# Kernel tuning notes

Measured on AMD Instinct MI355X. Metric: run time of the kernel, lower is better.

The kernel has to match this reference:

```python
import jax, jax.numpy as jnp
import numpy as np
from jax import lax

# dims: batch, seq len, views, d_model; d_state, d_inner=2*d_model, d_conv, dt_rank=ceil(d_model/16)
B, L, V, D = 4, 512, 4, 256
DS, DI, DCONV, DTR = 16, 512, 4, 16
EPS = 1e-5

def setup_inputs():
    key = jax.random.key(0)
    ks = jax.random.split(key, 10)
    rn = lambda k, s, sc: jax.random.normal(k, s, jnp.float32) * sc
    return {
        "x": rn(ks[0], (B, L, V, D), 1.0),
        "ln_g": jnp.ones((V, D), jnp.float32),
        "ln_b": jnp.zeros((V, D), jnp.float32),
        "w_in": rn(ks[1], (V, 2 * DI, D), D ** -0.5),
        "conv_w": rn(ks[2], (V, DI, DCONV), DCONV ** -0.5),
        "conv_b": rn(ks[3], (V, DI), 0.02),
        "w_x": rn(ks[4], (V, DTR + 2 * DS, DI), DI ** -0.5),
        "w_dt": rn(ks[5], (V, DI, DTR), DTR ** -0.5),
        "b_dt": rn(ks[6], (V, DI), 0.02),
        "A_log": rn(ks[7], (V, DI, DS), 0.5),
        "D_skip": jnp.ones((V, DI), jnp.float32),
        "w_out": rn(ks[8], (V, D, DI), DI ** -0.5),
    }

def _layernorm(x, g, b):
    mu = x.mean(-1, keepdims=True)
    var = ((x - mu) ** 2).mean(-1, keepdims=True)
    return (x - mu) * lax.rsqrt(var + EPS) * g + b

def _mamba_view(xv, w_in, conv_w, conv_b, w_x, w_dt, b_dt, A_log, D_skip, w_out):
    # xv: (B, L, D)
    xz = jnp.einsum('bld,ed->ble', xv, w_in)            # (B, L, 2*DI)
    xi, z = xz[..., :DI], xz[..., DI:]
    # causal depthwise conv over time
    xt = jnp.moveaxis(xi, 1, 2)                          # (B, DI, L)
    xt = jnp.pad(xt, ((0, 0), (0, 0), (DCONV - 1, 0)))
    xc = lax.conv_general_dilated(xt, conv_w[:, None, :], (1,), 'VALID',
                                  feature_group_count=DI,
                                  dimension_numbers=('NCH', 'OIH', 'NCH'))
    xc = jax.nn.silu(xc + conv_b[None, :, None])
    xc = jnp.moveaxis(xc, 1, 2)                          # (B, L, DI)
    xdbl = jnp.einsum('bld,ed->ble', xc, w_x)            # (B, L, DTR+2*DS)
    dt_lo = xdbl[..., :DTR]
    Bc = xdbl[..., DTR:DTR + DS]
    Cc = xdbl[..., DTR + DS:]
    delta = jax.nn.softplus(jnp.einsum('blr,dr->bld', dt_lo, w_dt) + b_dt)
    A = -jnp.exp(A_log)                                  # (DI, DS)
    dA = jnp.exp(jnp.einsum('bld,dn->bldn', delta, A))   # discretized A
    dBu = jnp.einsum('bld,bln,bld->bldn', delta, Bc, xc) # discretized B*u

    def step(h, inp):
        dA_t, dBu_t, C_t = inp
        h = dA_t * h + dBu_t                             # (B, DI, DS)
        return h, jnp.einsum('bdn,bn->bd', h, C_t)

    h0 = jnp.zeros((B, DI, DS), xv.dtype)
    _, ys = lax.scan(step, h0, (jnp.moveaxis(dA, 1, 0), jnp.moveaxis(dBu, 1, 0), jnp.moveaxis(Cc, 1, 0)))
    y = jnp.moveaxis(ys, 0, 1) + xc * D_skip             # (B, L, DI)
    y = y * jax.nn.silu(z)
    return jnp.einsum('bld,od->blo', y, w_out)           # (B, L, D)

def _forward(x, ln_g, ln_b, w_in, conv_w, conv_b, w_x, w_dt, b_dt, A_log, D_skip, w_out):
    xv = jnp.moveaxis(x, 2, 0)                           # (V, B, L, D)
    def per_view(xv_i, g, b, wi, cw, cb, wx, wdt, bdt, al, dsk, wo):
        return _mamba_view(_layernorm(xv_i, g, b), wi, cw, cb, wx, wdt, bdt, al, dsk, wo)
    outs = jax.vmap(per_view)(xv, ln_g, ln_b, w_in, conv_w, conv_b, w_x, w_dt, b_dt, A_log, D_skip, w_out)
    return jnp.moveaxis(outs, 0, 2)                      # (B, L, V, D)

def reference(x, ln_g, ln_b, w_in, conv_w, conv_b, w_x, w_dt, b_dt, A_log, D_skip, w_out):
    # eval mode: view_mask == ones, dropout identity, gather is None -> h == agents
    agents = _forward(x, ln_g, ln_b, w_in, conv_w, conv_b, w_x, w_dt, b_dt, A_log, D_skip, w_out)
    return (agents, agents)
```

## Files before the change

### kernel.cpp

```cpp
#include <hip/hip_runtime.h>
#include <hip/hip_bf16.h>
#include <math.h>

#define B_ 4
#define L_ 512
#define V_ 4
#define D_ 256
#define DS_ 16
#define DI_ 512
#define DTR_ 16
#define ML (B_*L_)
#define NC_ 16
#define CL_ 32

#define OFF_RA   0
#define SZ_RA    ((long)V_*ML*D_)
#define OFF_XZ   (OFF_RA + SZ_RA)
#define SZ_XZ    ((long)V_*ML*2*DI_)
#define OFF_XC   (OFF_XZ + SZ_XZ)
#define SZ_XC    ((long)V_*ML*DI_)
#define OFF_XDBL (OFF_XC + SZ_XC)
#define SZ_XDBL  ((long)V_*ML*48)
#define OFF_SDEL (OFF_XDBL + SZ_XDBL)
#define SZ_SDEL  ((long)V_*B_*NC_*DI_)

typedef short short8_t __attribute__((ext_vector_type(8)));
typedef float f32x4_t  __attribute__((ext_vector_type(4)));

__device__ __forceinline__ float silu_f(float x) { return x / (1.f + expf(-x)); }
__device__ __forceinline__ ushort f2bf(float f) {
    uint u = __float_as_uint(f);
    return (ushort)((u + 0x7fffu + ((u >> 16) & 1u)) >> 16);
}
__device__ __forceinline__ float bf2f(ushort h) { return __uint_as_float(((uint)h) << 16); }

__global__ __launch_bounds__(256) void split_w(const float* __restrict__ in,
                                               ushort* __restrict__ oh,
                                               ushort* __restrict__ ol, int n4)
{
    const int i = blockIdx.x*256 + threadIdx.x;
    if (i >= n4) return;
    const float4 f = ((const float4*)in)[i];
    const ushort h0=f2bf(f.x), h1=f2bf(f.y), h2=f2bf(f.z), h3=f2bf(f.w);
    ((short4*)oh)[i] = make_short4((short)h0,(short)h1,(short)h2,(short)h3);
    ((short4*)ol)[i] = make_short4((short)f2bf(f.x-bf2f(h0)), (short)f2bf(f.y-bf2f(h1)),
                                   (short)f2bf(f.z-bf2f(h2)), (short)f2bf(f.w-bf2f(h3)));
}

__global__ __launch_bounds__(256) void ln_split(const float* __restrict__ x,
                                                const float* __restrict__ g,
                                                const float* __restrict__ bta,
                                                ushort* __restrict__ xh,
                                                ushort* __restrict__ xl)
{
    const int m = blockIdx.x;
    const int v = blockIdx.y;
    const int d = threadIdx.x;
    const float val = x[((long)m*V_ + v)*D_ + d];
    float s = val, sq = val*val;
#pragma unroll
    for (int off = 32; off >= 1; off >>= 1) {
        s  += __shfl_xor(s, off);
        sq += __shfl_xor(sq, off);
    }
    __shared__ float ws[4], wq[4];
    if ((threadIdx.x & 63) == 0) { ws[threadIdx.x >> 6] = s; wq[threadIdx.x >> 6] = sq; }
    __syncthreads();
    s  = ws[0]+ws[1]+ws[2]+ws[3];
    sq = wq[0]+wq[1]+wq[2]+wq[3];
    const float mu  = s * (1.f/D_);
    const float var = sq * (1.f/D_) - mu*mu;
    const float inv = rsqrtf(var + 1e-5f);
    const float r = (val - mu)*inv*g[v*D_+d] + bta[v*D_+d];
    const ushort h = f2bf(r);
    const long idx = ((long)v*ML + m)*D_ + d;
    xh[idx] = h;
    xl[idx] = f2bf(r - bf2f(h));
}

__global__ __launch_bounds__(256,2) void mfma_gemm_in(
    const ushort* __restrict__ Ah, const ushort* __restrict__ Al,
    const ushort* __restrict__ Bh, const ushort* __restrict__ Bl,
    float* __restrict__ C)
{
    const int v = blockIdx.z;
    const long Ao = (long)v*ML*D_;
    const long Bo = (long)v*(2*DI_)*D_;
    C += (long)v*ML*(2*DI_);
    const int bm = blockIdx.y*128, bn = blockIdx.x*128;
    __shared__ ushort sAh[128][40], sAl[128][40], sBh[128][40], sBl[128][40];
    const int tid  = threadIdx.x;
    const int lane = tid & 63, w = tid >> 6;
    const int wr = w >> 1, wc = w & 1;
    const int fm = lane & 15, fg = lane >> 4;
    const int r = tid >> 1, q0 = (tid & 1)*2;

    f32x4_t acc[4][4];
#pragma unroll
    for (int i=0;i<4;++i)
#pragma unroll
        for (int j=0;j<4;++j)
#pragma unroll
            for (int k=0;k<4;++k) acc[i][j][k]=0.f;

    const ushort* Agh = Ah + Ao + (long)(bm+r)*D_ + q0*8;
    const ushort* Agl = Al + Ao + (long)(bm+r)*D_ + q0*8;
    const ushort* Bgh = Bh + Bo + (long)(bn+r)*D_ + q0*8;
    const ushort* Bgl = Bl + Bo + (long)(bn+r)*D_ + q0*8;

    for (int k0 = 0; k0 < D_; k0 += 32) {
        const uint4 a0 = *(const uint4*)(Agh + k0);
        const uint4 a1 = *(const uint4*)(Agh + k0 + 8);
        const uint4 a2 = *(const uint4*)(Agl + k0);
        const uint4 a3 = *(const uint4*)(Agl + k0 + 8);
        const uint4 b0 = *(const uint4*)(Bgh + k0);
        const uint4 b1 = *(const uint4*)(Bgh + k0 + 8);
        const uint4 b2 = *(const uint4*)(Bgl + k0);
        const uint4 b3 = *(const uint4*)(Bgl + k0 + 8);
        __syncthreads();
        *(uint4*)&sAh[r][q0*8]   = a0;  *(uint4*)&sAh[r][q0*8+8] = a1;
        *(uint4*)&sAl[r][q0*8]   = a2;  *(uint4*)&sAl[r][q0*8+8] = a3;
        *(uint4*)&sBh[r][q0*8]   = b0;  *(uint4*)&sBh[r][q0*8+8] = b1;
        *(uint4*)&sBl[r][q0*8]   = b2;  *(uint4*)&sBl[r][q0*8+8] = b3;
        __syncthreads();
        short8_t ah[4], al[4], bh[4], bl[4];
#pragma unroll
        for (int i=0;i<4;++i) {
            ah[i] = *(const short8_t*)&sAh[wr*64 + i*16 + fm][fg*8];
            al[i] = *(const short8_t*)&sAl[wr*64 + i*16 + fm][fg*8];
            bh[i] = *(const short8_t*)&sBh[wc*64 + i*16 + fm][fg*8];
            bl[i] = *(const short8_t*)&sBl[wc*64 + i*16 + fm][fg*8];
        }
#pragma unroll
        for (int i=0;i<4;++i)
#pragma unroll
            for (int j=0;j<4;++j) {
                acc[i][j] = __builtin_amdgcn_mfma_f32_16x16x32_bf16(ah[i], bh[j], acc[i][j], 0,0,0);
                acc[i][j] = __builtin_amdgcn_mfma_f32_16x16x32_bf16(ah[i], bl[j], acc[i][j], 0,0,0);
                acc[i][j] = __builtin_amdgcn_mfma_f32_16x16x32_bf16(al[i], bh[j], acc[i][j], 0,0,0);
            }
    }
#pragma unroll
    for (int i=0;i<4;++i)
#pragma unroll
        for (int j4=0;j4<4;++j4) {
            const int row = bm + wr*64 + i*16 + fg*4 + j4;
            float* cr = C + (long)row*(2*DI_) + bn + wc*64 + fm;
#pragma unroll
            for (int j=0;j<4;++j) cr[j*16] = acc[i][j][j4];
        }
}

__global__ __launch_bounds__(256,2) void mfma_gemm_out(
    const uint* __restrict__ Apk,
    const ushort* __restrict__ Bh, const ushort* __restrict__ Bl,
    float* __restrict__ Cout)
{
    const int v = blockIdx.z;
    Apk += (long)v*ML*DI_;
    const long Bo = (long)v*D_*DI_;
    const int bm = blockIdx.y*128, bn = blockIdx.x*128;
    __shared__ ushort sAh[128][40], sAl[128][40], sBh[128][40], sBl[128][40];
    const int tid  = threadIdx.x;
    const int lane = tid & 63, w = tid >> 6;
    const int wr = w >> 1, wc = w & 1;
    const int fm = lane & 15, fg = lane >> 4;
    const int r = tid >> 1, hh = tid & 1, q0 = (tid & 1)*2;

    f32x4_t acc[4][4];
#pragma unroll
    for (int i=0;i<4;++i)
#pragma unroll
        for (int j=0;j<4;++j)
#pragma unroll
            for (int k=0;k<4;++k) acc[i][j][k]=0.f;

    const uint*   Ag  = Apk + (long)(bm+r)*DI_ + hh*16;
    const ushort* Bgh = Bh + Bo + (long)(bn+r)*DI_ + q0*8;
    const ushort* Bgl = Bl + Bo + (long)(bn+r)*DI_ + q0*8;

    for (int k0 = 0; k0 < DI_; k0 += 32) {
        const uint4 p0 = *(const uint4*)(Ag + k0);
        const uint4 p1 = *(const uint4*)(Ag + k0 + 4);
        const uint4 p2 = *(const uint4*)(Ag + k0 + 8);
        const uint4 p3 = *(const uint4*)(Ag + k0 + 12);
        const uint4 b0 = *(const uint4*)(Bgh + k0);
        const uint4 b1 = *(const uint4*)(Bgh + k0 + 8);
        const uint4 b2 = *(const uint4*)(Bgl + k0);
        const uint4 b3 = *(const uint4*)(Bgl + k0 + 8);
        __syncthreads();
        *(short4*)&sAh[r][hh*16+ 0] = make_short4((short)(p0.x&0xffff),(short)(p0.y&0xffff),(short)(p0.z&0xffff),(short)(p0.w&0xffff));
        *(short4*)&sAl[r][hh*16+ 0] = make_short4((short)(p0.x>>16),(short)(p0.y>>16),(short)(p0.z>>16),(short)(p0.w>>16));
        *(short4*)&sAh[r][hh*16+ 4] = make_short4((short)(p1.x&0xffff),(short)(p1.y&0xffff),(short)(p1.z&0xffff),(short)(p1.w&0xffff));
        *(short4*)&sAl[r][hh*16+ 4] = make_short4((short)(p1.x>>16),(short)(p1.y>>16),(short)(p1.z>>16),(short)(p1.w>>16));
        *(short4*)&sAh[r][hh*16+ 8] = make_short4((short)(p2.x&0xffff),(short)(p2.y&0xffff),(short)(p2.z&0xffff),(short)(p2.w&0xffff));
        *(short4*)&sAl[r][hh*16+ 8] = make_short4((short)(p2.x>>16),(short)(p2.y>>16),(short)(p2.z>>16),(short)(p2.w>>16));
        *(short4*)&sAh[r][hh*16+12] = make_short4((short)(p3.x&0xffff),(short)(p3.y&0xffff),(short)(p3.z&0xffff),(short)(p3.w&0xffff));
        *(short4*)&sAl[r][hh*16+12] = make_short4((short)(p3.x>>16),(short)(p3.y>>16),(short)(p3.z>>16),(short)(p3.w>>16));
        *(uint4*)&sBh[r][q0*8]   = b0;  *(uint4*)&sBh[r][q0*8+8] = b1;
        *(uint4*)&sBl[r][q0*8]   = b2;  *(uint4*)&sBl[r][q0*8+8] = b3;
        __syncthreads();
        short8_t ah[4], al[4], bh[4], bl[4];
#pragma unroll
        for (int i=0;i<4;++i) {
            ah[i] = *(const short8_t*)&sAh[wr*64 + i*16 + fm][fg*8];
            al[i] = *(const short8_t*)&sAl[wr*64 + i*16 + fm][fg*8];
            bh[i] = *(const short8_t*)&sBh[wc*64 + i*16 + fm][fg*8];
            bl[i] = *(const short8_t*)&sBl[wc*64 + i*16 + fm][fg*8];
        }
#pragma unroll
        for (int i=0;i<4;++i)
#pragma unroll
            for (int j=0;j<4;++j) {
                acc[i][j] = __builtin_amdgcn_mfma_f32_16x16x32_bf16(ah[i], bh[j], acc[i][j], 0,0,0);
                acc[i][j] = __builtin_amdgcn_mfma_f32_16x16x32_bf16(ah[i], bl[j], acc[i][j], 0,0,0);
                acc[i][j] = __builtin_amdgcn_mfma_f32_16x16x32_bf16(al[i], bh[j], acc[i][j], 0,0,0);
            }
    }
    const long TOT = (long)ML * V_ * D_;
#pragma unroll
    for (int i=0;i<4;++i)
#pragma unroll
        for (int j4=0;j4<4;++j4) {
            const int row = bm + wr*64 + i*16 + fg*4 + j4;
#pragma unroll
            for (int j=0;j<4;++j) {
                const int col = bn + wc*64 + j*16 + fm;
                const long base = ((long)row*V_ + v)*D_ + col;
                const float val = acc[i][j][j4];
                Cout[base]       = val;
                Cout[base + TOT] = val;
            }
        }
}

__global__ __launch_bounds__(512) void conv_silu(const float* __restrict__ xz,
                                                 const float* __restrict__ cw,
                                                 const float* __restrict__ cb,
                                                 float* __restrict__ xc)
{
    const int m = blockIdx.x;
    const int v = blockIdx.y;
    const int c = threadIdx.x;
    const int l = m & 511;
    const float* xzv = xz + (long)v*ML*2*DI_;
    const float4 w4 = *(const float4*)&cw[((long)v*DI_ + c)*4];
    const float w[4] = {w4.x, w4.y, w4.z, w4.w};
    float acc = cb[v*DI_ + c];
#pragma unroll
    for (int k = 0; k < 4; ++k) {
        const int lp = l - 3 + k;
        if (lp >= 0) acc = fmaf(xzv[(long)(m - 3 + k)*(2*DI_) + c], w[k], acc);
    }
    xc[((long)v*ML + m)*DI_ + c] = silu_f(acc);
}

__global__ __launch_bounds__(256) void gemm_nt48_sk(const float* __restrict__ A,
                                                    const float* __restrict__ Bm,
                                                    float* __restrict__ P,
                                                    long sAv, long sBv)
{
    const int v = blockIdx.z;
    const int ks = blockIdx.y;
    A  += (long)v * sAv;
    Bm += (long)v * sBv;
    P  += (long)v * ((long)ML*2*DI_);
    __shared__ float As[16][68];
    __shared__ float Bs[16][48];
    const int tid = threadIdx.x;
    const int tx = tid & 15, ty = tid >> 4;
    const int bm = blockIdx.x * 64;
    const int lr = tid >> 2;
    const int lk = (tid & 3) * 4;
    const float* Ag = A + (long)(bm + lr)*DI_ + lk;
    float acc[4][3] = {};
    for (int k0 = ks*128; k0 < ks*128 + 128; k0 += 16) {
        const float4 av = *(const float4*)(Ag + k0);
        float4 bv = {0,0,0,0};
        if (tid < 192) bv = *(const float4*)(Bm + (long)(tid >> 2)*DI_ + k0 + (tid & 3)*4);
        __syncthreads();
        As[lk+0][lr]=av.x; As[lk+1][lr]=av.y; As[lk+2][lr]=av.z; As[lk+3][lr]=av.w;
        if (tid < 192) {
            const int br = tid >> 2, bk = (tid & 3)*4;
            Bs[bk+0][br]=bv.x; Bs[bk+1][br]=bv.y; Bs[bk+2][br]=bv.z; Bs[bk+3][br]=bv.w;
        }
        __syncthreads();
#pragma unroll
        for (int kk = 0; kk < 16; ++kk) {
            const float4 a = *(const float4*)&As[kk][ty*4];
            const float b0 = Bs[kk][tx*3+0], b1 = Bs[kk][tx*3+1], b2 = Bs[kk][tx*3+2];
            acc[0][0]=fmaf(a.x,b0,acc[0][0]); acc[0][1]=fmaf(a.x,b1,acc[0][1]); acc[0][2]=fmaf(a.x,b2,acc[0][2]);
            acc[1][0]=fmaf(a.y,b0,acc[1][0]); acc[1][1]=fmaf(a.y,b1,acc[1][1]); acc[1][2]=fmaf(a.y,b2,acc[1][2]);
            acc[2][0]=fmaf(a.z,b0,acc[2][0]); acc[2][1]=fmaf(a.z,b1,acc[2][1]); acc[2][2]=fmaf(a.z,b2,acc[2][2]);
            acc[3][0]=fmaf(a.w,b0,acc[3][0]); acc[3][1]=fmaf(a.w,b1,acc[3][1]); acc[3][2]=fmaf(a.w,b2,acc[3][2]);
        }
    }
#pragma unroll
    for (int i = 0; i < 4; ++i)
#pragma unroll
        for (int j = 0; j < 3; ++j)
            P[(long)(bm + ty*4 + i)*(2*DI_) + ks*48 + tx*3 + j] = acc[i][j];
}

__global__ __launch_bounds__(256) void reduce48(const float* __restrict__ xz,
                                                float* __restrict__ xdbl)
{
    const long i = (long)blockIdx.x*256 + threadIdx.x;
    if (i >= (long)V_*ML*48) return;
    const long row = i / 48; const int j = (int)(i % 48);
    const float* p = xz + row*(2*DI_);
    xdbl[i] = (p[j] + p[48+j]) + (p[96+j] + p[144+j]);
}

__global__ __launch_bounds__(256) void scanA(const float* __restrict__ xcin,
                                             const float* __restrict__ xdbl,
                                             const float* __restrict__ A_log,
                                             const float* __restrict__ wdt,
                                             const float* __restrict__ bdt,
                                             float* __restrict__ hbuf,
                                             float* __restrict__ sdel)
{
    const int c = blockIdx.x >> 1, half = blockIdx.x & 1;
    const int b = blockIdx.y, v = blockIdx.z;
    const int d = half*256 + threadIdx.x;
    const long rowbase = (long)v*ML + (long)b*L_ + (long)c*CL_;
    const float* xcv = xcin + rowbase*DI_;
    const float* xdv = xdbl + rowbase*48;

    __shared__ float sX[CL_*48];
    for (int t = threadIdx.x; t < CL_*48; t += 256) sX[t] = xdv[t];

    float a2[16];
#pragma unroll
    for (int n = 0; n < 16; ++n)
        a2[n] = -expf(A_log[((long)v*DI_ + d)*DS_ + n]) * 1.44269504088896341f;
    float wreg[16];
    {
        const float* wp = wdt + ((long)v*DI_ + d)*DTR_;
#pragma unroll
        for (int r = 0; r < 16; r += 4) {
            const float4 t4 = *(const float4*)(wp + r);
            wreg[r]=t4.x; wreg[r+1]=t4.y; wreg[r+2]=t4.z; wreg[r+3]=t4.w;
        }
    }
    const float bias = bdt[(long)v*DI_ + d];
    float h[16];
#pragma unroll
    for (int n = 0; n < 16; ++n) h[n] = 0.f;
    float sdsum = 0.f;
    __syncthreads();

    float xcur[8], xnxt[8];
#pragma unroll
    for (int s = 0; s < 8; ++s) xcur[s] = xcv[(long)s*DI_ + d];

    for (int g = 0; g < CL_; g += 8) {
        if (g + 8 < CL_) {
#pragma unroll
            for (int s = 0; s < 8; ++s) xnxt[s] = xcv[(long)(g+8+s)*DI_ + d];
        }
#pragma unroll
        for (int s = 0; s < 8; ++s) {
            const float* xrow = &sX[(g+s)*48];
            float acc = bias;
#pragma unroll
            for (int r = 0; r < 16; ++r) acc = fmaf(xrow[r], wreg[r], acc);
            const float delta = fmaxf(acc, 0.f) + log1pf(expf(-fabsf(acc)));
            const float t1 = delta * xcur[s];
            sdsum += delta;
#pragma unroll
            for (int n = 0; n < 16; ++n)
                h[n] = fmaf(exp2f(delta*a2[n]), h[n], t1*xrow[16+n]);
        }
#pragma unroll
        for (int s = 0; s < 8; ++s) xcur[s] = xnxt[s];
    }
    float* hb = hbuf + ((((long)v*B_ + b)*NC_ + c)*DI_ + d)*16;
#pragma unroll
    for (int n = 0; n < 16; n += 4) {
        float4 r; r.x = h[n]; r.y = h[n+1]; r.z = h[n+2]; r.w = h[n+3];
        *(float4*)&hb[n] = r;
    }
    sdel[(((long)v*B_ + b)*NC_ + c)*DI_ + d] = sdsum;
}

__global__ __launch_bounds__(256) void scanB(const float* __restrict__ A_log,
                                             const float* __restrict__ sdel,
                                             float* __restrict__ hbuf)
{
    const long lin = (long)blockIdx.x*256 + threadIdx.x;
    const int n = (int)(lin & 15);
    const int d = (int)((lin >> 4) & 511);
    const int b = (int)((lin >> 13) & 3);
    const int v = (int)(lin >> 15);
    const float a2 = -expf(A_log[((long)v*DI_ + d)*DS_ + n]) * 1.44269504088896341f;
    float h = 0.f;
    long hidx = ((long)(v*B_ + b)*NC_)*DI_*16 + (long)d*16 + n;
    long sidx = ((long)(v*B_ + b)*NC_)*DI_ + d;
#pragma unroll
    for (int c = 0; c < NC_; ++c) {
        const float he = hbuf[hidx];
        const float P  = exp2f(a2 * sdel[sidx]);
        hbuf[hidx] = h;
        h = fmaf(P, h, he);
        hidx += (long)DI_*16;
        sidx += DI_;
    }
}

__global__ __launch_bounds__(256) void scanC(const float* __restrict__ xz,
                                             const float* __restrict__ xcin,
                                             const float* __restrict__ xdbl,
                                             const float* __restrict__ A_log,
                                             const float* __restrict__ wdt,
                                             const float* __restrict__ bdt,
                                             const float* __restrict__ D_skip,
                                             const float* __restrict__ hbuf,
                                             float* __restrict__ yout)
{
    const int c = blockIdx.x >> 1, half = blockIdx.x & 1;
    const int b = blockIdx.y, v = blockIdx.z;
    const int d = half*256 + threadIdx.x;
    const long rowbase = (long)v*ML + (long)b*L_ + (long)c*CL_;
    const float* xzv = xz   + rowbase*(2*DI_);
    const float* xcv = xcin + rowbase*DI_;
    const float* xdv = xdbl + rowbase*48;
    uint*        yv  = (uint*)yout + rowbase*DI_;

    __shared__ float sX[CL_*48];
    for (int t = threadIdx.x; t < CL_*48; t += 256) sX[t] = xdv[t];

    float a2[16];
#pragma unroll
    for (int n = 0; n < 16; ++n)
        a2[n] = -expf(A_log[((long)v*DI_ + d)*DS_ + n]) * 1.44269504088896341f;
    float wreg[16];
    {
        const float* wp = wdt + ((long)v*DI_ + d)*DTR_;
#pragma unroll
        for (int r = 0; r < 16; r += 4) {
            const float4 t4 = *(const float4*)(wp + r);
            wreg[r]=t4.x; wreg[r+1]=t4.y; wreg[r+2]=t4.z; wreg[r+3]=t4.w;
        }
    }
    const float bias = bdt[(long)v*DI_ + d];
    const float dsk = D_skip[v*DI_ + d];
    float h[16];
    const float* hb = hbuf + ((((long)v*B_ + b)*NC_ + c)*DI_ + d)*16;
#pragma unroll
    for (int n = 0; n < 16; n += 4) {
        const float4 r = *(const float4*)&hb[n];
        h[n] = r.x; h[n+1] = r.y; h[n+2] = r.z; h[n+3] = r.w;
    }
    __syncthreads();

    float xcur[8], zcur[8], xnxt[8], znxt[8];
#pragma unroll
    for (int s = 0; s < 8; ++s) {
        xcur[s] = xcv[(long)s*DI_ + d];
        zcur[s] = xzv[(long)s*(2*DI_) + DI_ + d];
    }

    for (int g = 0; g < CL_; g += 8) {
        if (g + 8 < CL_) {
#pragma unroll
            for (int s = 0; s < 8; ++s) {
                xnxt[s] = xcv[(long)(g+8+s)*DI_ + d];
                znxt[s] = xzv[(long)(g+8+s)*(2*DI_) + DI_ + d];
            }
        }
#pragma unroll
        for (int s = 0; s < 8; ++s) {
            const float* xrow = &sX[(g+s)*48];
            float acc = bias;
#pragma unroll
            for (int r = 0; r < 16; ++r) acc = fmaf(xrow[r], wreg[r], acc);
            const float delta = fmaxf(acc, 0.f) + log1pf(expf(-fabsf(acc)));
            const float xcval = xcur[s];
            const float t1 = delta * xcval;
            float ys = 0.f;
#pragma unroll
            for (int n = 0; n < 16; ++n) {
                const float e = exp2f(delta*a2[n]);
                h[n] = fmaf(e, h[n], t1*xrow[16+n]);
                ys   = fmaf(h[n], xrow[32+n], ys);
            }
            float outv = ys + xcval * dsk;
            outv *= silu_f(zcur[s]);
            const ushort hv = f2bf(outv);
            const ushort lv = f2bf(outv - bf2f(hv));
            yv[(long)(g+s)*DI_ + d] = (uint)hv | ((uint)lv << 16);
        }
#pragma unroll
        for (int s = 0; s < 8; ++s) { xcur[s] = xnxt[s]; zcur[s] = znxt[s]; }
    }
}

extern "C" void kernel_launch(void* const* d_in, const int* in_sizes, int n_in,
                              void* d_out, int out_size, void* d_ws, size_t ws_size,
                              hipStream_t stream)
{
    const float* x      = (const float*)d_in[0];
    const float* ln_g   = (const float*)d_in[1];
    const float* ln_b   = (const float*)d_in[2];
    const float* w_in   = (const float*)d_in[3];
    const float* conv_w = (const float*)d_in[4];
    const float* conv_b = (const float*)d_in[5];
    const float* w_x    = (const float*)d_in[6];
    const float* w_dt   = (const float*)d_in[7];
    const float* b_dt   = (const float*)d_in[8];
    const float* A_log  = (const float*)d_in[9];
    const float* D_skip = (const float*)d_in[10];
    const float* w_out  = (const float*)d_in[11];
    float* out = (float*)d_out;

    float* ws   = (float*)d_ws;
    float* xz   = ws + OFF_XZ;
    float* xc   = ws + OFF_XC;
    float* xdbl = ws + OFF_XDBL;
    float* sdel = ws + OFF_SDEL;
    float* hbuf = ws + OFF_RA;

    ushort* xlnh = (ushort*)(ws + OFF_RA);
    ushort* xlnl = xlnh + (long)V_*ML*D_;
    ushort* wih = (ushort*)(ws + OFF_XC);
    ushort* wil = wih + (long)V_*(2*DI_)*D_;
    ushort* woh = (ushort*)(ws + OFF_RA);
    ushort* wol = woh + (long)V_*D_*DI_;

    split_w<<<dim3((V_*(2*DI_)*D_/4 + 255)/256), 256, 0, stream>>>(w_in, wih, wil, V_*(2*DI_)*D_/4);

    ln_split<<<dim3(ML, V_), 256, 0, stream>>>(x, ln_g, ln_b, xlnh, xlnl);

    mfma_gemm_in<<<dim3((2*DI_)/128, ML/128, V_), 256, 0, stream>>>(xlnh, xlnl, wih, wil, xz);

    conv_silu<<<dim3(ML, V_), DI_, 0, stream>>>(xz, conv_w, conv_b, xc);

    gemm_nt48_sk<<<dim3(ML/64, 4, V_), 256, 0, stream>>>(
        xc, w_x, xz, (long)ML*DI_, (long)48*DI_);
    reduce48<<<dim3((V_*ML*48 + 255)/256), 256, 0, stream>>>(xz, xdbl);

    scanA<<<dim3(NC_*2, B_, V_), 256, 0, stream>>>(xc, xdbl, A_log, w_dt, b_dt, hbuf, sdel);
    scanB<<<dim3((V_*B_*DI_*DS_)/256), 256, 0, stream>>>(A_log, sdel, hbuf);
    scanC<<<dim3(NC_*2, B_, V_), 256, 0, stream>>>(xz, xc, xdbl, A_log, w_dt, b_dt,
                                                   D_skip, hbuf, xc);

    split_w<<<dim3((V_*D_*DI_/4 + 255)/256), 256, 0, stream>>>(w_out, woh, wol, V_*D_*DI_/4);

    mfma_gemm_out<<<dim3(D_/128, ML/128, V_), 256, 0, stream>>>((const uint*)xc, woh, wol, out);
}
```

Measured before the change: 266.0 us.

## Halve scan chunk length, use fast exp/log intrinsics, reuse xz for chunk states

```diff
diff --git a/kernel.cpp b/kernel.cpp
--- a/kernel.cpp
+++ b/kernel.cpp
@@ -10,8 +10,8 @@
 #define DI_ 512
 #define DTR_ 16
 #define ML (B_*L_)
-#define NC_ 16
-#define CL_ 32
+#define NC_ 32
+#define CL_ 16
 
 #define OFF_RA   0
 #define SZ_RA    ((long)V_*ML*D_)
@@ -21,18 +21,33 @@
 #define SZ_XC    ((long)V_*ML*DI_)
 #define OFF_XDBL (OFF_XC + SZ_XC)
 #define SZ_XDBL  ((long)V_*ML*48)
-#define OFF_SDEL (OFF_XDBL + SZ_XDBL)
-#define SZ_SDEL  ((long)V_*B_*NC_*DI_)
 
 typedef short short8_t __attribute__((ext_vector_type(8)));
 typedef float f32x4_t  __attribute__((ext_vector_type(4)));
 
-__device__ __forceinline__ float silu_f(float x) { return x / (1.f + expf(-x)); }
+#define LOG2E 1.44269504088896341f
+#define LN2   0.69314718055994531f
+
+__device__ __forceinline__ float exp2_fast(float x) { return __builtin_amdgcn_exp2f(x); }
+__device__ __forceinline__ float softplus_fast(float x) {
+    const float t = __builtin_amdgcn_exp2f(x * LOG2E);
+    const float r = __builtin_amdgcn_logf(1.f + t) * LN2;
+    return x > 20.f ? x : r;
+}
+__device__ __forceinline__ float silu_fast(float z) {
+    const float t = __builtin_amdgcn_exp2f(-LOG2E * z);
+    return z * __builtin_amdgcn_rcpf(1.f + t);
+}
 __device__ __forceinline__ ushort f2bf(float f) {
     uint u = __float_as_uint(f);
     return (ushort)((u + 0x7fffu + ((u >> 16) & 1u)) >> 16);
 }
 __device__ __forceinline__ float bf2f(ushort h) { return __uint_as_float(((uint)h) << 16); }
+
+__device__ __forceinline__ long hb_idx(int v, int b, int c, int d) {
+    const long s = ((((long)b*NC_ + c)*DI_ + d) << 4);
+    return (long)v*ML*(2*DI_) + (s >> 9)*(2*DI_) + (s & 511);
+}
 
 __global__ __launch_bounds__(256) void split_w(const float* __restrict__ in,
                                                ushort* __restrict__ oh,
@@ -252,7 +267,7 @@
         const int lp = l - 3 + k;
         if (lp >= 0) acc = fmaf(xzv[(long)(m - 3 + k)*(2*DI_) + c], w[k], acc);
     }
-    xc[((long)v*ML + m)*DI_ + c] = silu_f(acc);
+    xc[((long)v*ML + m)*DI_ + c] = silu_fast(acc);
 }
 
 __global__ __launch_bounds__(256) void gemm_nt48_sk(const float* __restrict__ A,
@@ -317,7 +332,7 @@
                                              const float* __restrict__ A_log,
                                              const float* __restrict__ wdt,
                                              const float* __restrict__ bdt,
-                                             float* __restrict__ hbuf,
+                                             float* __restrict__ hxz,
                                              float* __restrict__ sdel)
 {
     const int c = blockIdx.x >> 1, half = blockIdx.x & 1;
@@ -333,7 +348,7 @@
     float a2[16];
 #pragma unroll
     for (int n = 0; n < 16; ++n)
-        a2[n] = -expf(A_log[((long)v*DI_ + d)*DS_ + n]) * 1.44269504088896341f;
+        a2[n] = -exp2_fast(A_log[((long)v*DI_ + d)*DS_ + n] * LOG2E) * LOG2E;
     float wreg[16];
     {
         const float* wp = wdt + ((long)v*DI_ + d)*DTR_;
@@ -362,20 +377,35 @@
 #pragma unroll
         for (int s = 0; s < 8; ++s) {
             const float* xrow = &sX[(g+s)*48];
+            const float4 t0 = *(const float4*)&xrow[0];
+            const float4 t1 = *(const float4*)&xrow[4];
+            const float4 t2 = *(const float4*)&xrow[8];
+            const float4 t3 = *(const float4*)&xrow[12];
             float acc = bias;
-#pragma unroll
-            for (int r = 0; r < 16; ++r) acc = fmaf(xrow[r], wreg[r], acc);
-            const float delta = fmaxf(acc, 0.f) + log1pf(expf(-fabsf(acc)));
-            const float t1 = delta * xcur[s];
+            acc = fmaf(t0.x,wreg[0],acc);  acc = fmaf(t0.y,wreg[1],acc);
+            acc = fmaf(t0.z,wreg[2],acc);  acc = fmaf(t0.w,wreg[3],acc);
+            acc = fmaf(t1.x,wreg[4],acc);  acc = fmaf(t1.y,wreg[5],acc);
+            acc = fmaf(t1.z,wreg[6],acc);  acc = fmaf(t1.w,wreg[7],acc);
+            acc = fmaf(t2.x,wreg[8],acc);  acc = fmaf(t2.y,wreg[9],acc);
+            acc = fmaf(t2.z,wreg[10],acc); acc = fmaf(t2.w,wreg[11],acc);
+            acc = fmaf(t3.x,wreg[12],acc); acc = fmaf(t3.y,wreg[13],acc);
+            acc = fmaf(t3.z,wreg[14],acc); acc = fmaf(t3.w,wreg[15],acc);
+            const float delta = softplus_fast(acc);
+            const float tx = delta * xcur[s];
             sdsum += delta;
 #pragma unroll
-            for (int n = 0; n < 16; ++n)
-                h[n] = fmaf(exp2f(delta*a2[n]), h[n], t1*xrow[16+n]);
+            for (int n4 = 0; n4 < 4; ++n4) {
+                const float4 Bv = *(const float4*)&xrow[16 + n4*4];
+                h[n4*4+0] = fmaf(exp2_fast(delta*a2[n4*4+0]), h[n4*4+0], tx*Bv.x);
+                h[n4*4+1] = fmaf(exp2_fast(delta*a2[n4*4+1]), h[n4*4+1], tx*Bv.y);
+                h[n4*4+2] = fmaf(exp2_fast(delta*a2[n4*4+2]), h[n4*4+2], tx*Bv.z);
+                h[n4*4+3] = fmaf(exp2_fast(delta*a2[n4*4+3]), h[n4*4+3], tx*Bv.w);
+            }
         }
 #pragma unroll
         for (int s = 0; s < 8; ++s) xcur[s] = xnxt[s];
     }
-    float* hb = hbuf + ((((long)v*B_ + b)*NC_ + c)*DI_ + d)*16;
+    float* hb = hxz + hb_idx(v, b, c, d);
 #pragma unroll
     for (int n = 0; n < 16; n += 4) {
         float4 r; r.x = h[n]; r.y = h[n+1]; r.z = h[n+2]; r.w = h[n+3];
@@ -386,24 +416,24 @@
 
 __global__ __launch_bounds__(256) void scanB(const float* __restrict__ A_log,
                                              const float* __restrict__ sdel,
-                                             float* __restrict__ hbuf)
+                                             float* __restrict__ hxz)
 {
     const long lin = (long)blockIdx.x*256 + threadIdx.x;
     const int n = (int)(lin & 15);
     const int d = (int)((lin >> 4) & 511);
     const int b = (int)((lin >> 13) & 3);
     const int v = (int)(lin >> 15);
-    const float a2 = -expf(A_log[((long)v*DI_ + d)*DS_ + n]) * 1.44269504088896341f;
+    const float a2 = -exp2_fast(A_log[((long)v*DI_ + d)*DS_ + n] * LOG2E) * LOG2E;
     float h = 0.f;
-    long hidx = ((long)(v*B_ + b)*NC_)*DI_*16 + (long)d*16 + n;
+    long hidx = hb_idx(v, b, 0, d) + n;
     long sidx = ((long)(v*B_ + b)*NC_)*DI_ + d;
 #pragma unroll
     for (int c = 0; c < NC_; ++c) {
-        const float he = hbuf[hidx];
-        const float P  = exp2f(a2 * sdel[sidx]);
-        hbuf[hidx] = h;
+        const float he = hxz[hidx];
+        const float P  = exp2_fast(a2 * sdel[sidx]);
+        hxz[hidx] = h;
         h = fmaf(P, h, he);
-        hidx += (long)DI_*16;
+        hidx += (long)16*(2*DI_);
         sidx += DI_;
     }
 }
@@ -415,7 +445,6 @@
                                              const float* __restrict__ wdt,
                                              const float* __restrict__ bdt,
                                              const float* __restrict__ D_skip,
-                                             const float* __restrict__ hbuf,
                                              float* __restrict__ yout)
 {
     const int c = blockIdx.x >> 1, half = blockIdx.x & 1;
@@ -433,7 +462,7 @@
     float a2[16];
 #pragma unroll
     for (int n = 0; n < 16; ++n)
-        a2[n] = -expf(A_log[((long)v*DI_ + d)*DS_ + n]) * 1.44269504088896341f;
+        a2[n] = -exp2_fast(A_log[((long)v*DI_ + d)*DS_ + n] * LOG2E) * LOG2E;
     float wreg[16];
     {
         const float* wp = wdt + ((long)v*DI_ + d)*DTR_;
@@ -446,7 +475,7 @@
     const float bias = bdt[(long)v*DI_ + d];
     const float dsk = D_skip[v*DI_ + d];
     float h[16];
-    const float* hb = hbuf + ((((long)v*B_ + b)*NC_ + c)*DI_ + d)*16;
+    const float* hb = xz + hb_idx(v, b, c, d);
 #pragma unroll
     for (int n = 0; n < 16; n += 4) {
         const float4 r = *(const float4*)&hb[n];
@@ -472,21 +501,38 @@
 #pragma unroll
         for (int s = 0; s < 8; ++s) {
             const float* xrow = &sX[(g+s)*48];
+            const float4 t0 = *(const float4*)&xrow[0];
+            const float4 t1 = *(const float4*)&xrow[4];
+            const float4 t2 = *(const float4*)&xrow[8];
+            const float4 t3 = *(const float4*)&xrow[12];
             float acc = bias;
-#pragma unroll
-            for (int r = 0; r < 16; ++r) acc = fmaf(xrow[r], wreg[r], acc);
-            const float delta = fmaxf(acc, 0.f) + log1pf(expf(-fabsf(acc)));
+            acc = fmaf(t0.x,wreg[0],acc);  acc = fmaf(t0.y,wreg[1],acc);
+            acc = fmaf(t0.z,wreg[2],acc);  acc = fmaf(t0.w,wreg[3],acc);
+            acc = fmaf(t1.x,wreg[4],acc);  acc = fmaf(t1.y,wreg[5],acc);
+            acc = fmaf(t1.z,wreg[6],acc);  acc = fmaf(t1.w,wreg[7],acc);
+            acc = fmaf(t2.x,wreg[8],acc);  acc = fmaf(t2.y,wreg[9],acc);
+            acc = fmaf(t2.z,wreg[10],acc); acc = fmaf(t2.w,wreg[11],acc);
+            acc = fmaf(t3.x,wreg[12],acc); acc = fmaf(t3.y,wreg[13],acc);
+            acc = fmaf(t3.z,wreg[14],acc); acc = fmaf(t3.w,wreg[15],acc);
+            const float delta = softplus_fast(acc);
             const float xcval = xcur[s];
-            const float t1 = delta * xcval;
+            const float tx = delta * xcval;
             float ys = 0.f;
 #pragma unroll
-            for (int n = 0; n < 16; ++n) {
-                const float e = exp2f(delta*a2[n]);
-                h[n] = fmaf(e, h[n], t1*xrow[16+n]);
-                ys   = fmaf(h[n], xrow[32+n], ys);
+            for (int n4 = 0; n4 < 4; ++n4) {
+                const float4 Bv = *(const float4*)&xrow[16 + n4*4];
+                const float4 Cv = *(const float4*)&xrow[32 + n4*4];
+                h[n4*4+0] = fmaf(exp2_fast(delta*a2[n4*4+0]), h[n4*4+0], tx*Bv.x);
+                h[n4*4+1] = fmaf(exp2_fast(delta*a2[n4*4+1]), h[n4*4+1], tx*Bv.y);
+                h[n4*4+2] = fmaf(exp2_fast(delta*a2[n4*4+2]), h[n4*4+2], tx*Bv.z);
+                h[n4*4+3] = fmaf(exp2_fast(delta*a2[n4*4+3]), h[n4*4+3], tx*Bv.w);
+                ys = fmaf(h[n4*4+0], Cv.x, ys);
+                ys = fmaf(h[n4*4+1], Cv.y, ys);
+                ys = fmaf(h[n4*4+2], Cv.z, ys);
+                ys = fmaf(h[n4*4+3], Cv.w, ys);
             }
             float outv = ys + xcval * dsk;
-            outv *= silu_f(zcur[s]);
+            outv *= silu_fast(zcur[s]);
             const ushort hv = f2bf(outv);
             const ushort lv = f2bf(outv - bf2f(hv));
             yv[(long)(g+s)*DI_ + d] = (uint)hv | ((uint)lv << 16);
@@ -518,8 +564,7 @@
     float* xz   = ws + OFF_XZ;
     float* xc   = ws + OFF_XC;
     float* xdbl = ws + OFF_XDBL;
-    float* sdel = ws + OFF_SDEL;
-    float* hbuf = ws + OFF_RA;
+    float* sdel = ws + OFF_RA;
 
     ushort* xlnh = (ushort*)(ws + OFF_RA);
     ushort* xlnl = xlnh + (long)V_*ML*D_;
@@ -540,10 +585,10 @@
         xc, w_x, xz, (long)ML*DI_, (long)48*DI_);
     reduce48<<<dim3((V_*ML*48 + 255)/256), 256, 0, stream>>>(xz, xdbl);
 
-    scanA<<<dim3(NC_*2, B_, V_), 256, 0, stream>>>(xc, xdbl, A_log, w_dt, b_dt, hbuf, sdel);
-    scanB<<<dim3((V_*B_*DI_*DS_)/256), 256, 0, stream>>>(A_log, sdel, hbuf);
+    scanA<<<dim3(NC_*2, B_, V_), 256, 0, stream>>>(xc, xdbl, A_log, w_dt, b_dt, xz, sdel);
+    scanB<<<dim3((V_*B_*DI_*DS_)/256), 256, 0, stream>>>(A_log, sdel, xz);
     scanC<<<dim3(NC_*2, B_, V_), 256, 0, stream>>>(xz, xc, xdbl, A_log, w_dt, b_dt,
-                                                   D_skip, hbuf, xc);
+                                                   D_skip, xc);
 
     split_w<<<dim3((V_*D_*DI_/4 + 255)/256), 256, 0, stream>>>(w_out, woh, wol, V_*D_*DI_/4);
 
```

Measured after the change: 228.2 us. -14.2%, faster.
